# Optimization experiments

Measured on AMD Instinct MI355X. Metric: run time of the kernel, lower is better.

## Reference

```python
import jax, jax.numpy as jnp
import numpy as np

D_MODEL = 1024
D_STATE = 16
D_CONV = 4
EXPAND = 2
D_INNER = EXPAND * D_MODEL          # 2048
DT_RANK = D_MODEL // 16             # 64 ('auto' in mamba_ssm)
B_SZ = 2
SEQ = 1024


def setup_inputs() -> dict:
    key = jax.random.key(0)
    ks = jax.random.split(key, 8)
    g = lambda k, shape, scale: (jax.random.normal(k, shape, dtype=jnp.float32) * scale)
    x = jax.random.normal(ks[0], (B_SZ, SEQ, D_MODEL), dtype=jnp.float32)
    in_proj_w = g(ks[1], (2 * D_INNER, D_MODEL), D_MODEL ** -0.5)
    conv_w = g(ks[2], (D_INNER, 1, D_CONV), D_CONV ** -0.5)
    conv_b = jnp.zeros((D_INNER,), jnp.float32)
    x_proj_w = g(ks[3], (DT_RANK + 2 * D_STATE, D_INNER), D_INNER ** -0.5)
    dt_proj_w = g(ks[4], (D_INNER, DT_RANK), DT_RANK ** -0.5)
    # dt bias initialized so softplus(bias) ~ [1e-3, 0.1] like mamba_ssm
    dt_proj_b = jax.random.uniform(ks[5], (D_INNER,), jnp.float32, -6.0, -2.0)
    # S4D-real init: A = -(1..d_state) per channel
    A_log = jnp.log(jnp.tile(jnp.arange(1, D_STATE + 1, dtype=jnp.float32), (D_INNER, 1)))
    D = jnp.ones((D_INNER,), jnp.float32)
    out_proj_w = g(ks[6], (D_MODEL, D_INNER), D_INNER ** -0.5)
    return dict(x=x, in_proj_w=in_proj_w, conv_w=conv_w, conv_b=conv_b,
                x_proj_w=x_proj_w, dt_proj_w=dt_proj_w, dt_proj_b=dt_proj_b,
                A_log=A_log, D=D, out_proj_w=out_proj_w)


def _mamba(x, in_proj_w, conv_w, conv_b, x_proj_w, dt_proj_w, dt_proj_b, A_log, D, out_proj_w):
    Bt, L, _ = x.shape
    # input projection -> [B, L, 2*d_inner], split into conv branch u and gate z
    xz = jnp.einsum('bld,ed->ble', x, in_proj_w)
    u, z = jnp.split(xz, 2, axis=-1)
    # causal depthwise conv1d over time
    uc = jnp.transpose(u, (0, 2, 1))  # [B, d_inner, L]
    uc = jax.lax.conv_general_dilated(
        uc, conv_w, window_strides=(1,), padding=[(D_CONV - 1, 0)],
        feature_group_count=D_INNER, dimension_numbers=('NCH', 'OIH', 'NCH'))
    u = jax.nn.silu(jnp.transpose(uc, (0, 2, 1)) + conv_b)  # [B, L, d_inner]
    # data-dependent SSM parameters
    x_dbl = jnp.einsum('bld,ed->ble', u, x_proj_w)  # [B, L, dt_rank + 2*d_state]
    dt, Bmat, Cmat = jnp.split(x_dbl, [DT_RANK, DT_RANK + D_STATE], axis=-1)
    delta = jax.nn.softplus(jnp.einsum('blr,dr->bld', dt, dt_proj_w) + dt_proj_b)
    A = -jnp.exp(A_log)  # [d_inner, d_state], strictly negative

    def step(h, inp):
        d_t, B_t, C_t, u_t = inp  # [B,d_inner],[B,d_state],[B,d_state],[B,d_inner]
        dA = jnp.exp(d_t[:, :, None] * A)                       # [B, d_inner, d_state]
        h = dA * h + (d_t * u_t)[:, :, None] * B_t[:, None, :]  # discretized update
        y = jnp.einsum('bdn,bn->bd', h, C_t)
        return h, y

    h0 = jnp.zeros((Bt, D_INNER, D_STATE), x.dtype)
    xs = (jnp.swapaxes(delta, 0, 1), jnp.swapaxes(Bmat, 0, 1),
          jnp.swapaxes(Cmat, 0, 1), jnp.swapaxes(u, 0, 1))
    _, ys = jax.lax.scan(step, h0, xs)
    y = jnp.swapaxes(ys, 0, 1) + u * D   # skip connection D*u
    y = y * jax.nn.silu(z)               # gated output
    return jnp.einsum('bld,ed->ble', y, out_proj_w)


def reference(x, in_proj_w, conv_w, conv_b, x_proj_w, dt_proj_w, dt_proj_b, A_log, D, out_proj_w):
    # ResidualMamba: x + Mamba(x)
    return x + _mamba(x, in_proj_w, conv_w, conv_b, x_proj_w, dt_proj_w, dt_proj_b, A_log, D, out_proj_w)
```

## Files before the change

kernel.cpp:

```cpp
#include <hip/hip_runtime.h>
#include <hip/hip_bf16.h>
#include <math.h>

#define D_MODEL 1024
#define D_STATE 16
#define D_CONV  4
#define D_INNER 2048
#define DT_RANK 64
#define B_SZ    2
#define SEQ     1024
#define ML      (B_SZ * SEQ)

typedef unsigned short ushort_t;
typedef __attribute__((ext_vector_type(8))) short s8v;
typedef __attribute__((ext_vector_type(4))) float f4v;

__device__ __forceinline__ float softplus_f(float v) {
    return (v > 20.f) ? v : log1pf(__expf(v));
}

__global__ __launch_bounds__(256) void split_bf16_tiled(
    const float* __restrict__ A, ushort_t* __restrict__ H, ushort_t* __restrict__ L,
    int Kd, int ktlog, int total)
{
    int t = blockIdx.x * 256 + threadIdx.x;
    if (t >= total) return;
    int kslot = t & 3;
    int r  = (t >> 2) & 127;
    int tl = t >> 9;
    int kt = tl & ((1 << ktlog) - 1);
    int rt = tl >> ktlog;
    int row = rt * 128 + r;
    int col = (kt << 5) + kslot * 8;

    const float* src = &A[(size_t)row * Kd + col];
    float4 v0 = *reinterpret_cast<const float4*>(src);
    float4 v1 = *reinterpret_cast<const float4*>(src + 4);
    float f[8] = {v0.x, v0.y, v0.z, v0.w, v1.x, v1.y, v1.z, v1.w};
    s8v hv, lv;
#pragma unroll
    for (int j = 0; j < 8; ++j) {
        unsigned int ub = __float_as_uint(f[j]);
        unsigned int hb = (ub + 0x7fffu + ((ub >> 16) & 1u)) >> 16;
        float hf = __uint_as_float(hb << 16);
        float g  = f[j] - hf;
        unsigned int ug = __float_as_uint(g);
        unsigned int lb = (ug + 0x7fffu + ((ug >> 16) & 1u)) >> 16;
        hv[j] = (short)hb;
        lv[j] = (short)lb;
    }
    *reinterpret_cast<s8v*>(&H[(size_t)t * 8]) = hv;
    *reinterpret_cast<s8v*>(&L[(size_t)t * 8]) = lv;
}

template <int WTM, bool RES>
__global__ __launch_bounds__(256) void gemm_mfma_split(
    const ushort_t* __restrict__ Ah, const ushort_t* __restrict__ Al,
    const ushort_t* __restrict__ Bh, const ushort_t* __restrict__ Bl,
    const float* __restrict__ Rres,
    float* __restrict__ C, int ldc, int K)
{
    constexpr int BM  = WTM * 32;
    constexpr int CPW = BM / 64;
    __shared__ short AhL[BM * 32], AlL[BM * 32];
    __shared__ short BhL[128 * 32], BlL[128 * 32];

    const int tid = threadIdx.x;
    const int l = tid & 63;
    const int w = tid >> 6;
    const int m0 = blockIdx.y * BM;
    const int n0 = blockIdx.x * 128;
    const int wm = (w >> 1) * (WTM * 16);
    const int wn = (w & 1) * 64;

    const int ktiles = K >> 5;
    size_t abase = (size_t)(m0 >> 7) * ktiles * 4096 + (size_t)(m0 & 127) * 32;
    size_t bbase = (size_t)(n0 >> 7) * ktiles * 4096;

    f4v acc[WTM][4] = {};

    for (int kt = 0; kt < ktiles; ++kt) {
#pragma unroll
        for (int i = 0; i < CPW; ++i) {
            int ci = w * CPW + i;
            __builtin_amdgcn_global_load_lds(
                (const __attribute__((address_space(1))) unsigned int*)(Ah + abase + ci * 512 + l * 8),
                (__attribute__((address_space(3))) unsigned int*)&AhL[ci * 512], 16, 0, 0);
            __builtin_amdgcn_global_load_lds(
                (const __attribute__((address_space(1))) unsigned int*)(Al + abase + ci * 512 + l * 8),
                (__attribute__((address_space(3))) unsigned int*)&AlL[ci * 512], 16, 0, 0);
        }
#pragma unroll
        for (int i = 0; i < 2; ++i) {
            int ci = w * 2 + i;
            __builtin_amdgcn_global_load_lds(
                (const __attribute__((address_space(1))) unsigned int*)(Bh + bbase + ci * 512 + l * 8),
                (__attribute__((address_space(3))) unsigned int*)&BhL[ci * 512], 16, 0, 0);
            __builtin_amdgcn_global_load_lds(
                (const __attribute__((address_space(1))) unsigned int*)(Bl + bbase + ci * 512 + l * 8),
                (__attribute__((address_space(3))) unsigned int*)&BlL[ci * 512], 16, 0, 0);
        }
        asm volatile("s_waitcnt vmcnt(0)" ::: "memory");
        __syncthreads();

        s8v fah[WTM], fal[WTM], fbh[4], fbl[4];
        const int fo = (l & 15) * 32 + (l >> 4) * 8;
#pragma unroll
        for (int tr = 0; tr < WTM; ++tr) {
            fah[tr] = *reinterpret_cast<const s8v*>(&AhL[(wm + tr * 16) * 32 + fo]);
            fal[tr] = *reinterpret_cast<const s8v*>(&AlL[(wm + tr * 16) * 32 + fo]);
        }
#pragma unroll
        for (int tc = 0; tc < 4; ++tc) {
            fbh[tc] = *reinterpret_cast<const s8v*>(&BhL[(wn + tc * 16) * 32 + fo]);
            fbl[tc] = *reinterpret_cast<const s8v*>(&BlL[(wn + tc * 16) * 32 + fo]);
        }

#pragma unroll
        for (int tr = 0; tr < WTM; ++tr)
#pragma unroll
            for (int tc = 0; tc < 4; ++tc) {
                f4v c = acc[tr][tc];
                c = __builtin_amdgcn_mfma_f32_16x16x32_bf16(fah[tr], fbh[tc], c, 0, 0, 0);
                c = __builtin_amdgcn_mfma_f32_16x16x32_bf16(fah[tr], fbl[tc], c, 0, 0, 0);
                c = __builtin_amdgcn_mfma_f32_16x16x32_bf16(fal[tr], fbh[tc], c, 0, 0, 0);
                acc[tr][tc] = c;
            }
        __syncthreads();
        abase += 4096;
        bbase += 4096;
    }

    const int mb = m0 + wm + ((l >> 4) << 2);
    const int nb = n0 + wn + (l & 15);
#pragma unroll
    for (int tr = 0; tr < WTM; ++tr)
#pragma unroll
        for (int tc = 0; tc < 4; ++tc)
#pragma unroll
            for (int r = 0; r < 4; ++r) {
                int m = mb + tr * 16 + r;
                int n = nb + tc * 16;
                float v = acc[tr][tc][r];
                if (RES) v += Rres[(size_t)m * ldc + n];
                C[(size_t)m * ldc + n] = v;
            }
}

__global__ __launch_bounds__(256) void conv_silu(
    const float* __restrict__ xz,
    const float* __restrict__ cw,
    const float* __restrict__ cb,
    float* __restrict__ u)
{
    int idx = blockIdx.x * 256 + threadIdx.x;
    if (idx >= ML * (D_INNER / 4)) return;
    int d4  = idx & (D_INNER / 4 - 1);
    int row = idx >> 9;
    int l   = row & (SEQ - 1);

    const float* base = xz + (size_t)row * 4096 + d4 * 4;
    float xr[4][4];
    {
        float4 v = *reinterpret_cast<const float4*>(base);
        xr[0][0] = v.x; xr[0][1] = v.y; xr[0][2] = v.z; xr[0][3] = v.w;
    }
#pragma unroll
    for (int t = 1; t < 4; ++t) {
        float4 v = make_float4(0.f, 0.f, 0.f, 0.f);
        if (l >= t) v = *reinterpret_cast<const float4*>(base - (size_t)t * 4096);
        xr[t][0] = v.x; xr[t][1] = v.y; xr[t][2] = v.z; xr[t][3] = v.w;
    }
    float4 b4 = *reinterpret_cast<const float4*>(&cb[d4 * 4]);
    float bb[4] = {b4.x, b4.y, b4.z, b4.w};
    float out[4];
#pragma unroll
    for (int c = 0; c < 4; ++c) {
        float4 w = *reinterpret_cast<const float4*>(&cw[(d4 * 4 + c) * 4]);
        float s = bb[c];
        s = fmaf(w.w, xr[0][c], s);
        s = fmaf(w.z, xr[1][c], s);
        s = fmaf(w.y, xr[2][c], s);
        s = fmaf(w.x, xr[3][c], s);
        out[c] = s / (1.f + __expf(-s));
    }
    *reinterpret_cast<float4*>(&u[(size_t)row * 2048 + d4 * 4]) =
        make_float4(out[0], out[1], out[2], out[3]);
}

__global__ __launch_bounds__(256) void xproj_partial(
    const float* __restrict__ u,
    const float* __restrict__ W,
    float* __restrict__ part)
{
    __shared__ float Us[64][36];
    __shared__ float Ws[96][36];
    const int tid = threadIdx.x;
    const int tx = tid & 31;
    const int ty = tid >> 5;
    const int r0 = blockIdx.x * 64;
    const int kbase = blockIdx.y * 256;

    float acc[8][3] = {};

    for (int kc = kbase; kc < kbase + 256; kc += 32) {
#pragma unroll
        for (int i = 0; i < 2; ++i) {
            int f = tid + i * 256, row = f >> 3, kq = f & 7;
            *reinterpret_cast<float4*>(&Us[row][kq * 4]) =
                *reinterpret_cast<const float4*>(&u[(size_t)(r0 + row) * 2048 + kc + kq * 4]);
        }
#pragma unroll
        for (int i = 0; i < 3; ++i) {
            int f = tid + i * 256, row = f >> 3, kq = f & 7;
            *reinterpret_cast<float4*>(&Ws[row][kq * 4]) =
                *reinterpret_cast<const float4*>(&W[(size_t)row * 2048 + kc + kq * 4]);
        }
        __syncthreads();
#pragma unroll
        for (int k4 = 0; k4 < 32; k4 += 4) {
            float4 wv[3];
#pragma unroll
            for (int j = 0; j < 3; ++j)
                wv[j] = *reinterpret_cast<const float4*>(&Ws[tx + 32 * j][k4]);
#pragma unroll
            for (int i = 0; i < 8; ++i) {
                float4 uv = *reinterpret_cast<const float4*>(&Us[ty * 8 + i][k4]);
#pragma unroll
                for (int j = 0; j < 3; ++j) {
                    acc[i][j] = fmaf(uv.x, wv[j].x, acc[i][j]);
                    acc[i][j] = fmaf(uv.y, wv[j].y, acc[i][j]);
                    acc[i][j] = fmaf(uv.z, wv[j].z, acc[i][j]);
                    acc[i][j] = fmaf(uv.w, wv[j].w, acc[i][j]);
                }
            }
        }
        __syncthreads();
    }
#pragma unroll
    for (int i = 0; i < 8; ++i)
#pragma unroll
        for (int j = 0; j < 3; ++j)
            part[((size_t)blockIdx.y * ML + r0 + ty * 8 + i) * 96 + tx + 32 * j] = acc[i][j];
}

__global__ __launch_bounds__(256) void xproj_reduce(
    const float* __restrict__ part,
    float* __restrict__ xdbl)
{
    int i = blockIdx.x * 256 + threadIdx.x;
    if (i >= ML * 96 / 4) return;
    const float4* p4 = reinterpret_cast<const float4*>(part);
    float4 s = p4[i];
#pragma unroll
    for (int sgl = 1; sgl < 8; ++sgl) {
        float4 v = p4[(size_t)sgl * (ML * 96 / 4) + i];
        s.x += v.x; s.y += v.y; s.z += v.z; s.w += v.w;
    }
    reinterpret_cast<float4*>(xdbl)[i] = s;
}

#define CH 64

__global__ __launch_bounds__(256) void scan_kernel(
    const float* __restrict__ u,
    const float* __restrict__ xdbl,
    const float* __restrict__ xz,
    const float* __restrict__ A_log,
    const float* __restrict__ Dvec,
    const float* __restrict__ dtw,
    const float* __restrict__ dtb,
    float* __restrict__ yg)
{
    __shared__ __align__(16) float sdt[CH][68];
    __shared__ __align__(16) float sdel[16][CH + 4], su16[16][CH + 4],
                                   sB[16][CH + 4], sC[16][CH + 4];
    __shared__ __align__(16) float dtw_s[16][68];
    __shared__ float db_s[16];
    __shared__ __align__(16) float sy[CH][20];

    const int tid = threadIdx.x;
    const int b   = blockIdx.x >> 7;
    const int d0  = (blockIdx.x & 127) * 16;
    const int dch = tid >> 4;
    const int n   = tid & 15;

    const int sc4 = (tid & 3) * 4;
    const int slr = tid >> 2;

    {
        int r = tid >> 4, c4 = (tid & 15) * 4;
        *reinterpret_cast<float4*>(&dtw_s[r][c4]) =
            *reinterpret_cast<const float4*>(&dtw[(size_t)(d0 + r) * 64 + c4]);
        if (tid < 16) db_s[tid] = dtb[d0 + tid];
    }
    const float Aval = -expf(A_log[(d0 + dch) * 16 + n]);
    const float Dsel = (n == 15) ? Dvec[d0 + dch] : 0.f;
    float h = 0.f;
    __syncthreads();

    for (int l0 = 0; l0 < SEQ; l0 += CH) {
        {
#pragma unroll
            for (int i = 0; i < 4; ++i) {
                int idx = tid + i * 256;
                int rr = idx >> 4, c4 = (idx & 15) * 4;
                *reinterpret_cast<float4*>(&sdt[rr][c4]) =
                    *reinterpret_cast<const float4*>(&xdbl[(size_t)(b * SEQ + l0 + rr) * 96 + c4]);
            }
            int row = b * SEQ + l0 + slr;
            float4 uv = *reinterpret_cast<const float4*>(&u[(size_t)row * 2048 + d0 + sc4]);
            float4 Bv = *reinterpret_cast<const float4*>(&xdbl[(size_t)row * 96 + 64 + sc4]);
            float4 Cv = *reinterpret_cast<const float4*>(&xdbl[(size_t)row * 96 + 80 + sc4]);
            su16[sc4 + 0][slr] = uv.x; su16[sc4 + 1][slr] = uv.y;
            su16[sc4 + 2][slr] = uv.z; su16[sc4 + 3][slr] = uv.w;
            sB[sc4 + 0][slr] = Bv.x; sB[sc4 + 1][slr] = Bv.y;
            sB[sc4 + 2][slr] = Bv.z; sB[sc4 + 3][slr] = Bv.w;
            sC[sc4 + 0][slr] = Cv.x; sC[sc4 + 1][slr] = Cv.y;
            sC[sc4 + 2][slr] = Cv.z; sC[sc4 + 3][slr] = Cv.w;
        }
        __syncthreads();

        {
            float4 s0 = make_float4(0.f, 0.f, 0.f, 0.f), s1 = s0, s2 = s0, s3 = s0;
#pragma unroll
            for (int k4 = 0; k4 < 64; k4 += 4) {
                float4 dv = *reinterpret_cast<const float4*>(&sdt[slr][k4]);
                float4 w0 = *reinterpret_cast<const float4*>(&dtw_s[sc4 + 0][k4]);
                float4 w1 = *reinterpret_cast<const float4*>(&dtw_s[sc4 + 1][k4]);
                float4 w2 = *reinterpret_cast<const float4*>(&dtw_s[sc4 + 2][k4]);
                float4 w3 = *reinterpret_cast<const float4*>(&dtw_s[sc4 + 3][k4]);
                s0.x = fmaf(dv.x, w0.x, s0.x); s0.y = fmaf(dv.y, w0.y, s0.y);
                s0.z = fmaf(dv.z, w0.z, s0.z); s0.w = fmaf(dv.w, w0.w, s0.w);
                s1.x = fmaf(dv.x, w1.x, s1.x); s1.y = fmaf(dv.y, w1.y, s1.y);
                s1.z = fmaf(dv.z, w1.z, s1.z); s1.w = fmaf(dv.w, w1.w, s1.w);
                s2.x = fmaf(dv.x, w2.x, s2.x); s2.y = fmaf(dv.y, w2.y, s2.y);
                s2.z = fmaf(dv.z, w2.z, s2.z); s2.w = fmaf(dv.w, w2.w, s2.w);
                s3.x = fmaf(dv.x, w3.x, s3.x); s3.y = fmaf(dv.y, w3.y, s3.y);
                s3.z = fmaf(dv.z, w3.z, s3.z); s3.w = fmaf(dv.w, w3.w, s3.w);
            }
            sdel[sc4 + 0][slr] = softplus_f((s0.x + s0.y) + (s0.z + s0.w) + db_s[sc4 + 0]);
            sdel[sc4 + 1][slr] = softplus_f((s1.x + s1.y) + (s1.z + s1.w) + db_s[sc4 + 1]);
            sdel[sc4 + 2][slr] = softplus_f((s2.x + s2.y) + (s2.z + s2.w) + db_s[sc4 + 2]);
            sdel[sc4 + 3][slr] = softplus_f((s3.x + s3.y) + (s3.z + s3.w) + db_s[sc4 + 3]);
        }
        __syncthreads();

        float pbuf[8];
#pragma unroll 2
        for (int l8 = 0; l8 < CH; l8 += 8) {
#pragma unroll
            for (int g = 0; g < 2; ++g) {
                const int l4 = l8 + g * 4;
                float4 d4 = *reinterpret_cast<const float4*>(&sdel[dch][l4]);
                float4 u4 = *reinterpret_cast<const float4*>(&su16[dch][l4]);
                float4 B4 = *reinterpret_cast<const float4*>(&sB[n][l4]);
                float4 C4 = *reinterpret_cast<const float4*>(&sC[n][l4]);
                float dts[4] = {d4.x, d4.y, d4.z, d4.w};
                float uus[4] = {u4.x, u4.y, u4.z, u4.w};
                float Bs4[4] = {B4.x, B4.y, B4.z, B4.w};
                float Cs4[4] = {C4.x, C4.y, C4.z, C4.w};
#pragma unroll
                for (int j = 0; j < 4; ++j) {
                    float dt = dts[j];
                    float dA = __expf(dt * Aval);
                    h = fmaf(dA, h, dt * uus[j] * Bs4[j]);
                    pbuf[g * 4 + j] = fmaf(uus[j], Dsel, h * Cs4[j]);
                }
            }
#pragma unroll
            for (int j = 0; j < 8; ++j) {
                float p = pbuf[j];
                p += __int_as_float(__builtin_amdgcn_update_dpp(0, __float_as_int(p), 0x111, 0xf, 0xf, true));
                p += __int_as_float(__builtin_amdgcn_update_dpp(0, __float_as_int(p), 0x112, 0xf, 0xf, true));
                p += __int_as_float(__builtin_amdgcn_update_dpp(0, __float_as_int(p), 0x114, 0xf, 0xf, true));
                p += __int_as_float(__builtin_amdgcn_update_dpp(0, __float_as_int(p), 0x118, 0xf, 0xf, true));
                pbuf[j] = p;
            }
            if (n == 15) {
#pragma unroll
                for (int j = 0; j < 8; ++j) sy[l8 + j][dch] = pbuf[j];
            }
        }
        __syncthreads();

        {
            int row = b * SEQ + l0 + slr;
            float4 ps = *reinterpret_cast<const float4*>(&sy[slr][sc4]);
            float4 zv = *reinterpret_cast<const float4*>(&xz[(size_t)row * 4096 + 2048 + d0 + sc4]);
            float o[4];
            float pp[4] = {ps.x, ps.y, ps.z, ps.w};
            float zzv[4] = {zv.x, zv.y, zv.z, zv.w};
#pragma unroll
            for (int q = 0; q < 4; ++q) {
                float zz = zzv[q];
                o[q] = pp[q] * (zz / (1.f + __expf(-zz)));
            }
            *reinterpret_cast<float4*>(&yg[(size_t)row * 2048 + d0 + sc4]) =
                make_float4(o[0], o[1], o[2], o[3]);
        }
        __syncthreads();
    }
}

extern "C" void kernel_launch(void* const* d_in, const int* in_sizes, int n_in,
                              void* d_out, int out_size, void* d_ws, size_t ws_size,
                              hipStream_t stream)
{
    const float* x         = (const float*)d_in[0];
    const float* in_proj_w = (const float*)d_in[1];
    const float* conv_w    = (const float*)d_in[2];
    const float* conv_b    = (const float*)d_in[3];
    const float* x_proj_w  = (const float*)d_in[4];
    const float* dt_proj_w = (const float*)d_in[5];
    const float* dt_proj_b = (const float*)d_in[6];
    const float* A_log     = (const float*)d_in[7];
    const float* Dvec      = (const float*)d_in[8];
    const float* out_proj_w= (const float*)d_in[9];
    float* out = (float*)d_out;

    float* ws    = (float*)d_ws;
    float* xz    = ws;
    float* u     = ws + 8388608;
    float* xdbl  = ws + 12582912;
    float* part  = ws + 12779520;
    float* yg    = ws + 16973824;

    ushort_t* bfb = (ushort_t*)(ws + 21168128);
    ushort_t* Xh  = bfb;
    ushort_t* Xl  = bfb + 2097152;
    ushort_t* Wih = bfb + 4194304;
    ushort_t* Wil = bfb + 8388608;
    ushort_t* Ygh = bfb;
    ushort_t* Ygl = bfb + 4194304;
    ushort_t* Woh = bfb + 8388608;
    ushort_t* Wol = bfb + 10485760;

    split_bf16_tiled<<<dim3(1024), 256, 0, stream>>>(x, Xh, Xl, 1024, 5, ML * 1024 / 8);
    split_bf16_tiled<<<dim3(2048), 256, 0, stream>>>(in_proj_w, Wih, Wil, 1024, 5, 4096 * 1024 / 8);

    gemm_mfma_split<4, false><<<dim3(32, 16), 256, 0, stream>>>(
        Xh, Xl, Wih, Wil, nullptr, xz, 4096, 1024);

    conv_silu<<<dim3(ML * (D_INNER / 4) / 256), 256, 0, stream>>>(xz, conv_w, conv_b, u);

    xproj_partial<<<dim3(32, 8), 256, 0, stream>>>(u, x_proj_w, part);
    xproj_reduce<<<dim3((ML * 96 / 4 + 255) / 256), 256, 0, stream>>>(part, xdbl);

    scan_kernel<<<dim3(256), 256, 0, stream>>>(
        u, xdbl, xz, A_log, Dvec, dt_proj_w, dt_proj_b, yg);

    split_bf16_tiled<<<dim3(2048), 256, 0, stream>>>(yg, Ygh, Ygl, 2048, 6, ML * 2048 / 8);
    split_bf16_tiled<<<dim3(1024), 256, 0, stream>>>(out_proj_w, Woh, Wol, 2048, 6, 1024 * 2048 / 8);

    gemm_mfma_split<2, true><<<dim3(8, 32), 256, 0, stream>>>(
        Ygh, Ygl, Woh, Wol, x, out, 1024, 2048);
}
```

Measured before the change: 351.2 us.

## Split selective scan into two-pass segmented scan across sequence chunks

Replaces the single sequential scan kernel, which ran 256 blocks over the whole sequence, with a two-pass chunked scan over 8 sequence segments, launching 2048 blocks. Pass 1 computes delta, stores it to workspace, and records each segment's cumulative decay exponent and local end state. Pass 2 combines the states of earlier segments to get its starting state, then reruns the segment to produce outputs. The aim is to fill the GPU with more parallel work than 256 blocks provide. The cost is running the recurrence twice, an extra global write and read of delta, and a second launch.

```diff
diff --git a/kernel.cpp b/kernel.cpp
--- a/kernel.cpp
+++ b/kernel.cpp
@@ -261,30 +261,30 @@
 }
 
 #define CH 64
-
-__global__ __launch_bounds__(256) void scan_kernel(
+#define SEGP 8
+#define SEG (SEQ / SEGP)
+
+__global__ __launch_bounds__(256) void scan_pass1(
     const float* __restrict__ u,
     const float* __restrict__ xdbl,
-    const float* __restrict__ xz,
     const float* __restrict__ A_log,
-    const float* __restrict__ Dvec,
     const float* __restrict__ dtw,
     const float* __restrict__ dtb,
-    float* __restrict__ yg)
+    float* __restrict__ dl,
+    float2* __restrict__ segAB)
 {
     __shared__ __align__(16) float sdt[CH][68];
-    __shared__ __align__(16) float sdel[16][CH + 4], su16[16][CH + 4],
-                                   sB[16][CH + 4], sC[16][CH + 4];
+    __shared__ __align__(16) float sdel[16][CH + 4], su16[16][CH + 4], sB[16][CH + 4];
     __shared__ __align__(16) float dtw_s[16][68];
     __shared__ float db_s[16];
-    __shared__ __align__(16) float sy[CH][20];
 
     const int tid = threadIdx.x;
-    const int b   = blockIdx.x >> 7;
-    const int d0  = (blockIdx.x & 127) * 16;
+    const int bcg = blockIdx.x >> 3;
+    const int seg = blockIdx.x & 7;
+    const int b   = bcg >> 7;
+    const int d0  = (bcg & 127) * 16;
     const int dch = tid >> 4;
     const int n   = tid & 15;
-
     const int sc4 = (tid & 3) * 4;
     const int slr = tid >> 2;
 
@@ -295,11 +295,10 @@
         if (tid < 16) db_s[tid] = dtb[d0 + tid];
     }
     const float Aval = -expf(A_log[(d0 + dch) * 16 + n]);
-    const float Dsel = (n == 15) ? Dvec[d0 + dch] : 0.f;
-    float h = 0.f;
+    float h = 0.f, sAcc = 0.f;
     __syncthreads();
 
-    for (int l0 = 0; l0 < SEQ; l0 += CH) {
+    for (int l0 = seg * SEG; l0 < seg * SEG + SEG; l0 += CH) {
         {
 #pragma unroll
             for (int i = 0; i < 4; ++i) {
@@ -311,13 +310,10 @@
             int row = b * SEQ + l0 + slr;
             float4 uv = *reinterpret_cast<const float4*>(&u[(size_t)row * 2048 + d0 + sc4]);
             float4 Bv = *reinterpret_cast<const float4*>(&xdbl[(size_t)row * 96 + 64 + sc4]);
-            float4 Cv = *reinterpret_cast<const float4*>(&xdbl[(size_t)row * 96 + 80 + sc4]);
             su16[sc4 + 0][slr] = uv.x; su16[sc4 + 1][slr] = uv.y;
             su16[sc4 + 2][slr] = uv.z; su16[sc4 + 3][slr] = uv.w;
             sB[sc4 + 0][slr] = Bv.x; sB[sc4 + 1][slr] = Bv.y;
             sB[sc4 + 2][slr] = Bv.z; sB[sc4 + 3][slr] = Bv.w;
-            sC[sc4 + 0][slr] = Cv.x; sC[sc4 + 1][slr] = Cv.y;
-            sC[sc4 + 2][slr] = Cv.z; sC[sc4 + 3][slr] = Cv.w;
         }
         __syncthreads();
 
@@ -339,10 +335,86 @@
                 s3.x = fmaf(dv.x, w3.x, s3.x); s3.y = fmaf(dv.y, w3.y, s3.y);
                 s3.z = fmaf(dv.z, w3.z, s3.z); s3.w = fmaf(dv.w, w3.w, s3.w);
             }
-            sdel[sc4 + 0][slr] = softplus_f((s0.x + s0.y) + (s0.z + s0.w) + db_s[sc4 + 0]);
-            sdel[sc4 + 1][slr] = softplus_f((s1.x + s1.y) + (s1.z + s1.w) + db_s[sc4 + 1]);
-            sdel[sc4 + 2][slr] = softplus_f((s2.x + s2.y) + (s2.z + s2.w) + db_s[sc4 + 2]);
-            sdel[sc4 + 3][slr] = softplus_f((s3.x + s3.y) + (s3.z + s3.w) + db_s[sc4 + 3]);
+            float v0 = softplus_f((s0.x + s0.y) + (s0.z + s0.w) + db_s[sc4 + 0]);
+            float v1 = softplus_f((s1.x + s1.y) + (s1.z + s1.w) + db_s[sc4 + 1]);
+            float v2 = softplus_f((s2.x + s2.y) + (s2.z + s2.w) + db_s[sc4 + 2]);
+            float v3 = softplus_f((s3.x + s3.y) + (s3.z + s3.w) + db_s[sc4 + 3]);
+            sdel[sc4 + 0][slr] = v0; sdel[sc4 + 1][slr] = v1;
+            sdel[sc4 + 2][slr] = v2; sdel[sc4 + 3][slr] = v3;
+            int row = b * SEQ + l0 + slr;
+            *reinterpret_cast<float4*>(&dl[(size_t)row * 2048 + d0 + sc4]) =
+                make_float4(v0, v1, v2, v3);
+        }
+        __syncthreads();
+
+#pragma unroll 2
+        for (int l4 = 0; l4 < CH; l4 += 4) {
+            float4 d4 = *reinterpret_cast<const float4*>(&sdel[dch][l4]);
+            float4 u4 = *reinterpret_cast<const float4*>(&su16[dch][l4]);
+            float4 B4 = *reinterpret_cast<const float4*>(&sB[n][l4]);
+            float dts[4] = {d4.x, d4.y, d4.z, d4.w};
+            float uus[4] = {u4.x, u4.y, u4.z, u4.w};
+            float Bs4[4] = {B4.x, B4.y, B4.z, B4.w};
+#pragma unroll
+            for (int j = 0; j < 4; ++j) {
+                float t = dts[j] * Aval;
+                sAcc += t;
+                h = fmaf(__expf(t), h, dts[j] * uus[j] * Bs4[j]);
+            }
+        }
+        __syncthreads();
+    }
+    segAB[(size_t)blockIdx.x * 256 + tid] = make_float2(sAcc, h);
+}
+
+__global__ __launch_bounds__(256) void scan_pass2(
+    const float* __restrict__ u,
+    const float* __restrict__ xdbl,
+    const float* __restrict__ xz,
+    const float* __restrict__ A_log,
+    const float* __restrict__ Dvec,
+    const float* __restrict__ dl,
+    const float2* __restrict__ segAB,
+    float* __restrict__ yg)
+{
+    __shared__ __align__(16) float sdel[16][CH + 4], su16[16][CH + 4],
+                                   sB[16][CH + 4], sC[16][CH + 4];
+    __shared__ __align__(16) float sy[CH][20];
+
+    const int tid = threadIdx.x;
+    const int bcg = blockIdx.x >> 3;
+    const int seg = blockIdx.x & 7;
+    const int b   = bcg >> 7;
+    const int d0  = (bcg & 127) * 16;
+    const int dch = tid >> 4;
+    const int n   = tid & 15;
+    const int sc4 = (tid & 3) * 4;
+    const int slr = tid >> 2;
+
+    const float Aval = -expf(A_log[(d0 + dch) * 16 + n]);
+    const float Dsel = (n == 15) ? Dvec[d0 + dch] : 0.f;
+
+    float h = 0.f;
+    for (int j = 0; j < seg; ++j) {
+        float2 ab = segAB[((size_t)(bcg * SEGP + j)) * 256 + tid];
+        h = fmaf(__expf(ab.x), h, ab.y);
+    }
+
+    for (int l0 = seg * SEG; l0 < seg * SEG + SEG; l0 += CH) {
+        {
+            int row = b * SEQ + l0 + slr;
+            float4 dv = *reinterpret_cast<const float4*>(&dl[(size_t)row * 2048 + d0 + sc4]);
+            float4 uv = *reinterpret_cast<const float4*>(&u[(size_t)row * 2048 + d0 + sc4]);
+            float4 Bv = *reinterpret_cast<const float4*>(&xdbl[(size_t)row * 96 + 64 + sc4]);
+            float4 Cv = *reinterpret_cast<const float4*>(&xdbl[(size_t)row * 96 + 80 + sc4]);
+            sdel[sc4 + 0][slr] = dv.x; sdel[sc4 + 1][slr] = dv.y;
+            sdel[sc4 + 2][slr] = dv.z; sdel[sc4 + 3][slr] = dv.w;
+            su16[sc4 + 0][slr] = uv.x; su16[sc4 + 1][slr] = uv.y;
+            su16[sc4 + 2][slr] = uv.z; su16[sc4 + 3][slr] = uv.w;
+            sB[sc4 + 0][slr] = Bv.x; sB[sc4 + 1][slr] = Bv.y;
+            sB[sc4 + 2][slr] = Bv.z; sB[sc4 + 3][slr] = Bv.w;
+            sC[sc4 + 0][slr] = Cv.x; sC[sc4 + 1][slr] = Cv.y;
+            sC[sc4 + 2][slr] = Cv.z; sC[sc4 + 3][slr] = Cv.w;
         }
         __syncthreads();
 
@@ -435,6 +507,8 @@
     ushort_t* Ygl = bfb + 4194304;
     ushort_t* Woh = bfb + 8388608;
     ushort_t* Wol = bfb + 10485760;
+    float*  dl     = (float*)bfb;
+    float2* segAB  = (float2*)(ws + 25362432);
 
     split_bf16_tiled<<<dim3(1024), 256, 0, stream>>>(x, Xh, Xl, 1024, 5, ML * 1024 / 8);
     split_bf16_tiled<<<dim3(2048), 256, 0, stream>>>(in_proj_w, Wih, Wil, 1024, 5, 4096 * 1024 / 8);
@@ -447,8 +521,10 @@
     xproj_partial<<<dim3(32, 8), 256, 0, stream>>>(u, x_proj_w, part);
     xproj_reduce<<<dim3((ML * 96 / 4 + 255) / 256), 256, 0, stream>>>(part, xdbl);
 
-    scan_kernel<<<dim3(256), 256, 0, stream>>>(
-        u, xdbl, xz, A_log, Dvec, dt_proj_w, dt_proj_b, yg);
+    scan_pass1<<<dim3(256 * SEGP), 256, 0, stream>>>(
+        u, xdbl, A_log, dt_proj_w, dt_proj_b, dl, segAB);
+    scan_pass2<<<dim3(256 * SEGP), 256, 0, stream>>>(
+        u, xdbl, xz, A_log, Dvec, dl, segAB, yg);
 
     split_bf16_tiled<<<dim3(2048), 256, 0, stream>>>(yg, Ygh, Ygl, 2048, 6, ML * 2048 / 8);
     split_bf16_tiled<<<dim3(1024), 256, 0, stream>>>(out_proj_w, Woh, Wol, 2048, 6, 1024 * 2048 / 8);
```

Result: slower. 364.3 us (+3.7%).
